# Performance work log

Hardware: AMD Instinct MI355X
Metric: run time of the kernel (lower is better)

Reference implementation:

```python
import jax, jax.numpy as jnp
import numpy as np

B, R, VIS, MM, E, ATT, D, V, MAXLEN = 128, 36, 2048, 1024, 512, 512, 1024, 10000, 20


def setup_inputs() -> dict:
    key = jax.random.key(0)
    ks = jax.random.split(key, 16)
    s = 0.02
    visual = jax.random.normal(ks[0], (B, R, VIS), jnp.float32)
    joint = jax.random.normal(ks[1], (B, MM), jnp.float32)
    captions = jax.random.randint(ks[2], (B, MAXLEN), 0, V)
    # torch code requires lengths sorted descending (prefix slicing)
    lengths = jnp.sort(jax.random.randint(ks[3], (B,), 1, MAXLEN + 1))[::-1].astype(jnp.int32)
    embed_W = (jax.random.normal(ks[4], (V, E), jnp.float32) * s).at[0].set(0.0)  # padding_idx=0
    Wih = jax.random.normal(ks[5], (4 * D, E + VIS), jnp.float32) * s
    bih = jnp.zeros((4 * D,), jnp.float32)
    Whh = jax.random.normal(ks[6], (4 * D, D), jnp.float32) * s
    bhh = jnp.zeros((4 * D,), jnp.float32)
    W_init_h = jax.random.normal(ks[7], (D, MM), jnp.float32) * s
    b_init_h = jnp.zeros((D,), jnp.float32)
    W_init_c = jax.random.normal(ks[8], (D, MM), jnp.float32) * s
    b_init_c = jnp.zeros((D,), jnp.float32)
    Wv = jax.random.normal(ks[9], (ATT, VIS), jnp.float32) * s
    Wh = jax.random.normal(ks[10], (ATT, D), jnp.float32) * s
    att_bias = jnp.zeros((R,), jnp.float32)
    Ww = jax.random.normal(ks[11], (1, ATT), jnp.float32) * s
    Wout = jax.random.normal(ks[12], (V, D), jnp.float32) * s
    bout = jnp.zeros((V,), jnp.float32)
    return dict(visual=visual, joint=joint, captions=captions, lengths=lengths, max_len=MAXLEN,
                embed_W=embed_W, Wih=Wih, bih=bih, Whh=Whh, bhh=bhh,
                W_init_h=W_init_h, b_init_h=b_init_h, W_init_c=W_init_c, b_init_c=b_init_c,
                Wv=Wv, Wh=Wh, att_bias=att_bias, Ww=Ww, Wout=Wout, bout=bout)


def reference(visual, joint, captions, lengths, max_len, embed_W, Wih, bih, Whh, bhh,
              W_init_h, b_init_h, W_init_c, b_init_c, Wv, Wh, att_bias, Ww, Wout, bout):
    T = max_len - 1  # python int -> static scan length
    # dropout treated as identity (eval mode)
    words_seq = embed_W[captions[:, :T]]            # [B, T, E]
    h0 = joint @ W_init_h.T + b_init_h              # [B, D]
    c0 = joint @ W_init_c.T + b_init_c
    feas0 = visual.mean(axis=1)                     # [B, VIS]  (step 0 context)
    att_fea = jnp.einsum('brv,av->bra', visual, Wv)  # precompute visual projection
    lens = lengths.astype(jnp.int32)

    def step(carry, xs):
        h, c = carry
        t, words = xs
        # attention over 36 regions (used only when t != 0)
        ah = h @ Wh.T                                                   # [B, A]
        full = jax.nn.relu(att_fea + ah[:, None, :] + att_bias[None, :, None])
        alpha = jax.nn.softmax(jnp.einsum('bra,a->br', full, Ww[0]), axis=-1)
        ctx = jnp.einsum('br,brv->bv', alpha, visual)
        feas = jnp.where(t == 0, feas0, ctx)
        x = jnp.concatenate([feas, words], axis=-1)                     # [B, VIS+E]
        gates = x @ Wih.T + bih + h @ Whh.T + bhh                       # [B, 4D]
        i_, f_, g_, o_ = jnp.split(gates, 4, axis=-1)
        c_new = jax.nn.sigmoid(f_) * c + jax.nn.sigmoid(i_) * jnp.tanh(g_)
        h_new = jax.nn.sigmoid(o_) * jnp.tanh(c_new)
        mask = (t < lens)[:, None]                                      # ragged mask == torch prefix slice
        out = h_new @ Wout.T + bout                                     # [B, V]
        return (jnp.where(mask, h_new, h), jnp.where(mask, c_new, c)), jnp.where(mask, out, 0.0)

    _, preds = jax.lax.scan(step, (h0, c0), (jnp.arange(T), jnp.swapaxes(words_seq, 0, 1)))
    return jnp.transpose(preds, (1, 0, 2))  # [B, T, V]
```

## Files before the change

### kernel.cpp

```cpp
#include <hip/hip_runtime.h>
#include <math.h>

#define B 128
#define R 36
#define VIS 2048
#define MM 1024
#define E 512
#define ATT 512
#define D 1024
#define V 10000
#define MAXLEN 20
#define T 19
#define G4 4096

typedef unsigned short bf16_t;
typedef __attribute__((ext_vector_type(8))) short short8;
typedef __attribute__((ext_vector_type(4))) float f32x4;
typedef __attribute__((ext_vector_type(4))) unsigned short ushort4v;

__device__ __forceinline__ bf16_t f2bf(float f) {
    unsigned u = __float_as_uint(f);
    u += 0x7fff + ((u >> 16) & 1);
    return (bf16_t)(u >> 16);
}
__device__ __forceinline__ float bf2f(bf16_t b) {
    return __uint_as_float(((unsigned)b) << 16);
}
__device__ __forceinline__ float sigmoidf_(float x) { return 1.0f / (1.0f + expf(-x)); }

__device__ __forceinline__ void stage16(const bf16_t* g, bf16_t* lds_wave_base, int lane) {
#if defined(__has_builtin) && __has_builtin(__builtin_amdgcn_global_load_lds)
    __builtin_amdgcn_global_load_lds(
        (const __attribute__((address_space(1))) void*)g,
        (__attribute__((address_space(3))) void*)lds_wave_base, 16, 0, 0);
#else
    *(short8*)(lds_wave_base + lane * 8) = *(const short8*)g;
#endif
}

template<int MODE>
__global__ __launch_bounds__(256) void mfma_gemm_lds(
    const bf16_t* __restrict__ A, const bf16_t* __restrict__ W,
    const float* __restrict__ bias, const int* __restrict__ lengths,
    float* __restrict__ C, int M, int N, int K, int ldc)
{
    __shared__ __align__(16) bf16_t As[128 * 32];
    __shared__ __align__(16) bf16_t Ws[128 * 32];
    const int tid = threadIdx.x;
    const int wave = tid >> 6, lane = tid & 63;
    const int wm = wave >> 1, wn = wave & 1;
    const int quad = lane >> 4, l16 = lane & 15;
    const int m0 = blockIdx.y * 128;
    const int n0 = blockIdx.x * 128;
    if (MODE == 2 && n0 >= N) return;

    int cnt = 128;
    if constexpr (MODE == 2) {
        const int tt = blockIdx.y;
        cnt = __syncthreads_count(tid < B && lengths[tid] > tt);
    }

    f32x4 acc[4][4];
    #pragma unroll
    for (int i = 0; i < 4; ++i)
        #pragma unroll
        for (int j = 0; j < 4; ++j)
            acc[i][j] = (f32x4){0.f, 0.f, 0.f, 0.f};

    for (int kk = 0; kk < K; kk += 32) {
        #pragma unroll
        for (int i = 0; i < 2; ++i) {
            int c = tid + i * 256;
            int row = c >> 2, seg = c & 3;
            int m = m0 + row; if (m >= M) m = M - 1;
            stage16(A + (size_t)m * K + kk + seg * 8, &As[(i * 256 + wave * 64) * 8], lane);
            int n = n0 + row; if (n >= N) n = N - 1;
            stage16(W + (size_t)n * K + kk + seg * 8, &Ws[(i * 256 + wave * 64) * 8], lane);
        }
        __syncthreads();
        short8 af[4], bfr[4];
        #pragma unroll
        for (int fm = 0; fm < 4; ++fm) {
            const int rt = (MODE == 2) ? fm * 2 + wm : wm * 4 + fm;
            if (MODE != 2 || rt * 16 < cnt)
                af[fm] = *(const short8*)&As[(rt * 16 + l16) * 32 + quad * 8];
        }
        #pragma unroll
        for (int fn = 0; fn < 4; ++fn)
            bfr[fn] = *(const short8*)&Ws[(wn * 64 + fn * 16 + l16) * 32 + quad * 8];
        #pragma unroll
        for (int fm = 0; fm < 4; ++fm) {
            const int rt = (MODE == 2) ? fm * 2 + wm : wm * 4 + fm;
            if (MODE == 2 && rt * 16 >= cnt) continue;
            #pragma unroll
            for (int fn = 0; fn < 4; ++fn)
                acc[fm][fn] = __builtin_amdgcn_mfma_f32_16x16x32_bf16(
                    af[fm], bfr[fn], acc[fm][fn], 0, 0, 0);
        }
        __syncthreads();
    }

    #pragma unroll
    for (int fm = 0; fm < 4; ++fm) {
        const int rt = (MODE == 2) ? fm * 2 + wm : wm * 4 + fm;
        #pragma unroll
        for (int fn = 0; fn < 4; ++fn) {
            #pragma unroll
            for (int r = 0; r < 4; ++r) {
                int m = m0 + rt * 16 + quad * 4 + r;
                int n = n0 + wn * 64 + fn * 16 + l16;
                if (m >= M || n >= N) continue;
                float v = acc[fm][fn][r];
                if (MODE == 0) {
                    if (bias) v += bias[n];
                    C[(size_t)m * ldc + n] = v;
                } else if (MODE == 2) {
                    int t = m >> 7, b = m & 127;
                    v = (t < lengths[b]) ? (v + bias[n]) : 0.f;
                    C[((size_t)b * T + t) * V + n] = v;
                } else {
                    ((bf16_t*)C)[(size_t)m * ldc + n] = f2bf(v);
                }
            }
        }
    }
}

__global__ __launch_bounds__(256) void gemv_ah(
    const float* __restrict__ hf, const bf16_t* __restrict__ Wh_bf,
    float* __restrict__ ah)
{
    __shared__ float hs[16 * D];
    const int tid = threadIdx.x;
    const int bg = blockIdx.x;
    const int ag = blockIdx.y;
    const float4* src = (const float4*)(hf + (size_t)bg * 16 * D);
    #pragma unroll
    for (int i = 0; i < 16; ++i)
        ((float4*)hs)[i * 256 + tid] = src[i * 256 + tid];
    __syncthreads();

    const int lane = tid & 63, wave = tid >> 6;
    const int a = ag * 64 + lane;
    const bf16_t* wr = Wh_bf + (size_t)a * D;
    const float* h0 = hs + (wave * 4 + 0) * D;
    const float* h1 = hs + (wave * 4 + 1) * D;
    const float* h2 = hs + (wave * 4 + 2) * D;
    const float* h3 = hs + (wave * 4 + 3) * D;
    float s0 = 0.f, s1 = 0.f, s2 = 0.f, s3 = 0.f;
    for (int k = 0; k < D; k += 8) {
        short8 wv = *(const short8*)(wr + k);
        #pragma unroll
        for (int j = 0; j < 8; ++j) {
            float w = bf2f((bf16_t)wv[j]);
            s0 = fmaf(w, h0[k + j], s0);
            s1 = fmaf(w, h1[k + j], s1);
            s2 = fmaf(w, h2[k + j], s2);
            s3 = fmaf(w, h3[k + j], s3);
        }
    }
    const int b = bg * 16 + wave * 4;
    ah[(size_t)(b + 0) * ATT + a] = s0;
    ah[(size_t)(b + 1) * ATT + a] = s1;
    ah[(size_t)(b + 2) * ATT + a] = s2;
    ah[(size_t)(b + 3) * ATT + a] = s3;
}

__global__ __launch_bounds__(256) void att_sc_p(
    const float* __restrict__ ah, const float* __restrict__ att_fea,
    const float* __restrict__ att_bias, const float* __restrict__ Ww,
    const bf16_t* __restrict__ P_bf, const float* __restrict__ wordsW,
    float* __restrict__ partial, int t)
{
    const int b = blockIdx.x, half = blockIdx.y, tid = threadIdx.x;
    __shared__ float ah_s[ATT];
    __shared__ float sc_s[64];
    __shared__ float alpha_s[R];
    const int wave = tid >> 6, lane = tid & 63;

    if (t > 0) {
        if (tid < 128) ((float4*)ah_s)[tid] = ((const float4*)(ah + (size_t)b * ATT))[tid];
        __syncthreads();
        for (int r = wave; r < R; r += 4) {
            float abv = att_bias[r];
            const float* af = att_fea + ((size_t)b * R + r) * ATT;
            float s = 0.f;
            for (int a = lane; a < ATT; a += 64) {
                float v = af[a] + ah_s[a] + abv;
                s = fmaf(fmaxf(v, 0.f), Ww[a], s);
            }
            #pragma unroll
            for (int off = 32; off; off >>= 1) s += __shfl_down(s, off);
            if (lane == 0) sc_s[r] = s;
        }
        __syncthreads();
        if (tid < 64) {
            float v = (tid < R) ? sc_s[tid] : -INFINITY;
            float m = v;
            #pragma unroll
            for (int off = 32; off; off >>= 1) m = fmaxf(m, __shfl_down(m, off));
            m = __shfl(m, 0);
            float e = (tid < R) ? expf(v - m) : 0.f;
            float ss = e;
            #pragma unroll
            for (int off = 32; off; off >>= 1) ss += __shfl_down(ss, off);
            ss = __shfl(ss, 0);
            if (tid < R) alpha_s[tid] = e / ss;
        }
        __syncthreads();
    }

    const int n0c = half * 2048 + tid * 8;
    float acc[8];
    #pragma unroll
    for (int j = 0; j < 8; ++j) acc[j] = 0.f;
    const bf16_t* Pb = P_bf + (size_t)b * R * G4 + n0c;
    #pragma unroll 4
    for (int r = 0; r < R; ++r) {
        float al = (t == 0) ? (1.0f / R) : alpha_s[r];
        short8 p = *(const short8*)(Pb + (size_t)r * G4);
        #pragma unroll
        for (int j = 0; j < 8; ++j)
            acc[j] = fmaf(al, bf2f((bf16_t)p[j]), acc[j]);
    }
    const float* wsl = wordsW + ((size_t)t * B + b) * G4 + n0c;
    float* po = partial + (size_t)b * G4 + n0c;
    float4 w0 = *(const float4*)(wsl);
    float4 w1 = *(const float4*)(wsl + 4);
    float4 o0 = { acc[0] + w0.x, acc[1] + w0.y, acc[2] + w0.z, acc[3] + w0.w };
    float4 o1 = { acc[4] + w1.x, acc[5] + w1.y, acc[6] + w1.z, acc[7] + w1.w };
    *(float4*)(po)     = o0;
    *(float4*)(po + 4) = o1;
}

__global__ __launch_bounds__(256) void whh_pack_k(
    const bf16_t* __restrict__ Whh, bf16_t* __restrict__ pk)
{
    int idx = blockIdx.x * 256 + threadIdx.x;
    int dt = idx >> 12, c = idx & 4095;
    int row = c & 31, qk = c >> 5;
    int rv = (row >> 3) * D + dt * 8 + (row & 7);
    *(short8*)(pk + ((size_t)dt << 15) + (size_t)c * 8) =
        *(const short8*)(Whh + (size_t)rv * D + qk * 8);
}

__global__ __launch_bounds__(256) void gates_lstm(
    const bf16_t* __restrict__ h_in,
    const bf16_t* __restrict__ Whh_pk,
    const float* __restrict__ bih, const float* __restrict__ bhh,
    const float* __restrict__ partial,
    const int* __restrict__ lengths,
    float* __restrict__ c_st,
    float* __restrict__ h_f32,
    bf16_t* __restrict__ h_out,
    bf16_t* __restrict__ hseq,
    int t)
{
    __shared__ __align__(16) bf16_t Ws[32 * 1024];
    const int tid = threadIdx.x;
    const int wave = tid >> 6, lane = tid & 63;
    const int quad = lane >> 4, l16 = lane & 15;
    const int d0 = blockIdx.x * 8;
    const int m0 = blockIdx.y * 64;
    const int gsel_ = l16 >> 3, dr = l16 & 7;

    const bf16_t* slab = Whh_pk + ((size_t)blockIdx.x << 15);
    #pragma unroll
    for (int i = 0; i < 16; ++i) {
        int c = i * 256 + tid;
        stage16(slab + (size_t)c * 8, &Ws[(i * 256 + wave * 64) * 8], lane);
    }

    const bf16_t* Ar = h_in + (size_t)(m0 + wave * 16 + l16) * D + quad * 8;

    f32x4 acc0 = (f32x4){0.f, 0.f, 0.f, 0.f};
    f32x4 acc1 = (f32x4){0.f, 0.f, 0.f, 0.f};
    __syncthreads();

    #pragma unroll 8
    for (int kt = 0; kt < 32; ++kt) {
        short8 af = *(const short8*)(Ar + kt * 32);
        const int cb = (kt * 4 + quad) * 32 * 8;
        short8 b0 = *(const short8*)&Ws[cb + l16 * 8];
        short8 b1 = *(const short8*)&Ws[cb + (16 + l16) * 8];
        acc0 = __builtin_amdgcn_mfma_f32_16x16x32_bf16(af, b0, acc0, 0, 0, 0);
        acc1 = __builtin_amdgcn_mfma_f32_16x16x32_bf16(af, b1, acc1, 0, 0, 0);
    }

    const int d = d0 + dr;
    const int col0 = gsel_ * D + d;
    const int col1 = (2 + gsel_) * D + d;
    const float bia0 = bih[col0] + bhh[col0];
    const float bia1 = bih[col1] + bhh[col1];

    #pragma unroll
    for (int r = 0; r < 4; ++r) {
        int m = m0 + wave * 16 + quad * 4 + r;
        size_t pb = (size_t)m * G4;
        float v0 = acc0[r] + bia0 + partial[pb + col0];
        float v1 = acc1[r] + bia1 + partial[pb + col1];
        float w0 = __shfl_xor(v0, 8);
        float w1 = __shfl_xor(v1, 8);
        float iv, fv, gv, ov;
        if (gsel_ == 0) { iv = v0; gv = v1; fv = w0; ov = w1; }
        else            { fv = v0; ov = v1; iv = w0; gv = w1; }
        float ig = sigmoidf_(iv), fg = sigmoidf_(fv);
        float gg = tanhf(gv),     og = sigmoidf_(ov);
        size_t off = (size_t)m * D + d;
        if (gsel_ == 0) {
            float c_old = c_st[off];
            float h_old = h_f32[off];
            float cn = fmaf(fg, c_old, ig * gg);
            float hn = og * tanhf(cn);
            bool msk = t < lengths[m];
            float cv = msk ? cn : c_old;
            float hv = msk ? hn : h_old;
            c_st[off] = cv;
            h_f32[off] = hv;
            bf16_t hb = f2bf(hv);
            h_out[off] = hb;
            hseq[((size_t)t * B + m) * D + d] = hb;
        }
    }
}

__global__ __launch_bounds__(256) void cast_bf16_k(
    const float* __restrict__ src, bf16_t* __restrict__ dst,
    int rows, int cols, int ld)
{
    int idx = blockIdx.x * 256 + threadIdx.x;
    int total = rows * (cols >> 2);
    if (idx >= total) return;
    int cq = cols >> 2;
    int r = idx / cq, c4 = (idx - r * cq) * 4;
    float4 v = *(const float4*)(src + (size_t)r * ld + c4);
    ushort4v o = { f2bf(v.x), f2bf(v.y), f2bf(v.z), f2bf(v.w) };
    *(ushort4v*)(dst + (size_t)r * cols + c4) = o;
}

__global__ __launch_bounds__(128) void embed_k(
    const int* __restrict__ captions, const float* __restrict__ embed_W,
    bf16_t* __restrict__ words_bf)
{
    int bt = blockIdx.x;
    int b = bt / T, t = bt - b * T;
    int tok = captions[b * MAXLEN + t];
    int i = threadIdx.x * 4;
    float4 v = *(const float4*)(embed_W + (size_t)tok * E + i);
    ushort4v o = { f2bf(v.x), f2bf(v.y), f2bf(v.z), f2bf(v.w) };
    *(ushort4v*)(words_bf + ((size_t)t * B + b) * E + i) = o;
}

extern "C" void kernel_launch(void* const* d_in, const int* in_sizes, int n_in,
                              void* d_out, int out_size, void* d_ws, size_t ws_size,
                              hipStream_t stream) {
    const float* visual   = (const float*)d_in[0];
    const float* joint    = (const float*)d_in[1];
    const int*   captions = (const int*)d_in[2];
    const int*   lengths  = (const int*)d_in[3];
    const float* embed_W  = (const float*)d_in[5];
    const float* Wih      = (const float*)d_in[6];
    const float* bih      = (const float*)d_in[7];
    const float* Whh      = (const float*)d_in[8];
    const float* bhh      = (const float*)d_in[9];
    const float* W_init_h = (const float*)d_in[10];
    const float* b_init_h = (const float*)d_in[11];
    const float* W_init_c = (const float*)d_in[12];
    const float* b_init_c = (const float*)d_in[13];
    const float* Wv       = (const float*)d_in[14];
    const float* Wh       = (const float*)d_in[15];
    const float* att_bias = (const float*)d_in[16];
    const float* Ww       = (const float*)d_in[17];
    const float* Wout     = (const float*)d_in[18];
    const float* bout     = (const float*)d_in[19];
    float* out = (float*)d_out;

    char* cur = (char*)d_ws;
    auto alloc = [&](size_t bytes) { char* p = cur; cur += (bytes + 15) & ~size_t(15); return p; };
    float*  att_fea  = (float*)alloc((size_t)B * R * ATT * 4);
    float*  wordsW   = (float*)alloc((size_t)T * B * G4 * 4);
    float*  partial  = (float*)alloc((size_t)B * G4 * 4);
    float*  hf       = (float*)alloc((size_t)B * D * 4);
    float*  c_st     = (float*)alloc((size_t)B * D * 4);
    float*  ah       = (float*)alloc((size_t)B * ATT * 4);
    bf16_t* words_bf = (bf16_t*)alloc((size_t)T * B * E * 2);
    bf16_t* h_ping0  = (bf16_t*)alloc((size_t)B * D * 2);
    bf16_t* h_ping1  = (bf16_t*)alloc((size_t)B * D * 2);
    bf16_t* hseq_bf  = (bf16_t*)alloc((size_t)T * B * D * 2);
    bf16_t* P_bf     = (bf16_t*)alloc((size_t)B * R * G4 * 2);
    bf16_t* visual_bf= (bf16_t*)alloc((size_t)B * R * VIS * 2);
    bf16_t* Wv_bf    = (bf16_t*)alloc((size_t)ATT * VIS * 2);
    bf16_t* Wh_bf    = (bf16_t*)alloc((size_t)ATT * D * 2);
    bf16_t* Whh_bf   = (bf16_t*)alloc((size_t)G4 * D * 2);
    bf16_t* Whh_pk   = (bf16_t*)alloc((size_t)G4 * D * 2);
    bf16_t* Wih_v_bf = (bf16_t*)alloc((size_t)G4 * VIS * 2);
    bf16_t* Wih_w_bf = (bf16_t*)alloc((size_t)G4 * E * 2);
    bf16_t* Wout_bf  = (bf16_t*)alloc((size_t)V * D * 2);
    bf16_t* joint_bf = (bf16_t*)alloc((size_t)B * MM * 2);
    bf16_t* Winh_bf  = (bf16_t*)alloc((size_t)D * MM * 2);
    bf16_t* Winc_bf  = (bf16_t*)alloc((size_t)D * MM * 2);

    auto cast = [&](const float* s, bf16_t* dst, int rows, int cols, int ld) {
        int total = rows * (cols >> 2);
        cast_bf16_k<<<(total + 255) / 256, 256, 0, stream>>>(s, dst, rows, cols, ld);
    };
    cast(visual, visual_bf, 1, B * R * VIS, B * R * VIS);
    cast(Wv,  Wv_bf,  ATT, VIS, VIS);
    cast(Wh,  Wh_bf,  ATT, D, D);
    cast(Whh, Whh_bf, G4, D, D);
    cast(Wih, Wih_v_bf, G4, VIS, VIS + E);
    cast(Wih + VIS, Wih_w_bf, G4, E, VIS + E);
    cast(Wout, Wout_bf, V, D, D);
    cast(joint, joint_bf, 1, B * MM, B * MM);
    cast(W_init_h, Winh_bf, 1, D * MM, D * MM);
    cast(W_init_c, Winc_bf, 1, D * MM, D * MM);

    whh_pack_k<<<(128 * 4096) / 256, 256, 0, stream>>>(Whh_bf, Whh_pk);
    embed_k<<<B * T, 128, 0, stream>>>(captions, embed_W, words_bf);

    mfma_gemm_lds<0><<<dim3(D / 128, B / 128), 256, 0, stream>>>(
        joint_bf, Winh_bf, b_init_h, nullptr, hf, B, D, MM, D);
    mfma_gemm_lds<0><<<dim3(D / 128, B / 128), 256, 0, stream>>>(
        joint_bf, Winc_bf, b_init_c, nullptr, c_st, B, D, MM, D);
    cast(hf, h_ping0, 1, B * D, B * D);

    mfma_gemm_lds<0><<<dim3(ATT / 128, (B * R) / 128), 256, 0, stream>>>(
        visual_bf, Wv_bf, nullptr, nullptr, att_fea, B * R, ATT, VIS, ATT);

    mfma_gemm_lds<0><<<dim3(G4 / 128, (T * B) / 128), 256, 0, stream>>>(
        words_bf, Wih_w_bf, nullptr, nullptr, wordsW, T * B, G4, E, G4);

    mfma_gemm_lds<3><<<dim3(G4 / 128, (B * R) / 128), 256, 0, stream>>>(
        visual_bf, Wih_v_bf, nullptr, nullptr, (float*)P_bf, B * R, G4, VIS, G4);

    bf16_t* h_buf[2] = { h_ping0, h_ping1 };
    for (int t = 0; t < T; ++t) {
        if (t > 0)
            gemv_ah<<<dim3(8, 8), 256, 0, stream>>>(hf, Wh_bf, ah);
        att_sc_p<<<dim3(B, 2), 256, 0, stream>>>(
            ah, att_fea, att_bias, Ww, P_bf, wordsW, partial, t);
        gates_lstm<<<dim3(D / 8, B / 64), 256, 0, stream>>>(
            h_buf[t & 1], Whh_pk, bih, bhh, partial, lengths,
            c_st, hf, h_buf[(t + 1) & 1], hseq_bf, t);
    }

    mfma_gemm_lds<2><<<dim3(80, (T * B) / 128), 256, 0, stream>>>(
        hseq_bf, Wout_bf, bout, lengths, out, T * B, V, D, V);
}
```

Baseline: 1.534 ms.

## Use MFMA for attention hidden projection, fuse casts and init GEMMs

Replaces the scalar fp32 gemv for h@Wh^T with an MFMA bf16 kernel that reads a pre-packed Wh slab staged into LDS and the bf16 hidden state directly. The ten cast launches become one fused cast kernel. The two init GEMMs for h0/c0 become one GEMM that also writes the bf16 copy of h0. The output GEMM skips staging A rows that the length mask zeroes anyway. These target per-step latency in the recurrent loop and launch overhead, at the cost of bf16 rounding of h in the attention projection.

Measured after the change: 1.269 ms. 17.3% less time.

```diff
diff --git a/kernel.cpp b/kernel.cpp
--- a/kernel.cpp
+++ b/kernel.cpp
@@ -42,7 +42,9 @@
 __global__ __launch_bounds__(256) void mfma_gemm_lds(
     const bf16_t* __restrict__ A, const bf16_t* __restrict__ W,
     const float* __restrict__ bias, const int* __restrict__ lengths,
-    float* __restrict__ C, int M, int N, int K, int ldc)
+    float* __restrict__ C, int M, int N, int K, int ldc,
+    const float* __restrict__ bias2, float* __restrict__ C2,
+    bf16_t* __restrict__ C3)
 {
     __shared__ __align__(16) bf16_t As[128 * 32];
     __shared__ __align__(16) bf16_t Ws[128 * 32];
@@ -72,8 +74,10 @@
         for (int i = 0; i < 2; ++i) {
             int c = tid + i * 256;
             int row = c >> 2, seg = c & 3;
-            int m = m0 + row; if (m >= M) m = M - 1;
-            stage16(A + (size_t)m * K + kk + seg * 8, &As[(i * 256 + wave * 64) * 8], lane);
+            if (MODE != 2 || (i * 64 + wave * 16) < cnt) {
+                int m = m0 + row; if (m >= M) m = M - 1;
+                stage16(A + (size_t)m * K + kk + seg * 8, &As[(i * 256 + wave * 64) * 8], lane);
+            }
             int n = n0 + row; if (n >= N) n = N - 1;
             stage16(W + (size_t)n * K + kk + seg * 8, &Ws[(i * 256 + wave * 64) * 8], lane);
         }
@@ -118,6 +122,14 @@
                     int t = m >> 7, b = m & 127;
                     v = (t < lengths[b]) ? (v + bias[n]) : 0.f;
                     C[((size_t)b * T + t) * V + n] = v;
+                } else if (MODE == 4) {
+                    if (n < D) {
+                        float v2 = v + bias[n];
+                        C[(size_t)m * D + n] = v2;
+                        C3[(size_t)m * D + n] = f2bf(v2);
+                    } else {
+                        C2[(size_t)m * D + (n - D)] = v + bias2[n - D];
+                    }
                 } else {
                     ((bf16_t*)C)[(size_t)m * ldc + n] = f2bf(v);
                 }
@@ -126,44 +138,44 @@
     }
 }
 
-__global__ __launch_bounds__(256) void gemv_ah(
-    const float* __restrict__ hf, const bf16_t* __restrict__ Wh_bf,
+__global__ __launch_bounds__(256) void mfma_ah(
+    const bf16_t* __restrict__ h_in,
+    const bf16_t* __restrict__ Wh_pk,
     float* __restrict__ ah)
 {
-    __shared__ float hs[16 * D];
+    __shared__ __align__(16) bf16_t Ws[32 * 1024];
     const int tid = threadIdx.x;
-    const int bg = blockIdx.x;
-    const int ag = blockIdx.y;
-    const float4* src = (const float4*)(hf + (size_t)bg * 16 * D);
-    #pragma unroll
-    for (int i = 0; i < 16; ++i)
-        ((float4*)hs)[i * 256 + tid] = src[i * 256 + tid];
+    const int wave = tid >> 6, lane = tid & 63;
+    const int quad = lane >> 4, l16 = lane & 15;
+    const int a0 = blockIdx.x * 32;
+    const int m0 = blockIdx.y * 64;
+
+    const bf16_t* slab = Wh_pk + ((size_t)blockIdx.x << 15);
+    #pragma unroll
+    for (int i = 0; i < 16; ++i) {
+        int c = i * 256 + tid;
+        stage16(slab + (size_t)c * 8, &Ws[(i * 256 + wave * 64) * 8], lane);
+    }
+    const bf16_t* Ar = h_in + (size_t)(m0 + wave * 16 + l16) * D + quad * 8;
+    f32x4 acc0 = (f32x4){0.f, 0.f, 0.f, 0.f};
+    f32x4 acc1 = (f32x4){0.f, 0.f, 0.f, 0.f};
     __syncthreads();
 
-    const int lane = tid & 63, wave = tid >> 6;
-    const int a = ag * 64 + lane;
-    const bf16_t* wr = Wh_bf + (size_t)a * D;
-    const float* h0 = hs + (wave * 4 + 0) * D;
-    const float* h1 = hs + (wave * 4 + 1) * D;
-    const float* h2 = hs + (wave * 4 + 2) * D;
-    const float* h3 = hs + (wave * 4 + 3) * D;
-    float s0 = 0.f, s1 = 0.f, s2 = 0.f, s3 = 0.f;
-    for (int k = 0; k < D; k += 8) {
-        short8 wv = *(const short8*)(wr + k);
-        #pragma unroll
-        for (int j = 0; j < 8; ++j) {
-            float w = bf2f((bf16_t)wv[j]);
-            s0 = fmaf(w, h0[k + j], s0);
-            s1 = fmaf(w, h1[k + j], s1);
-            s2 = fmaf(w, h2[k + j], s2);
-            s3 = fmaf(w, h3[k + j], s3);
-        }
-    }
-    const int b = bg * 16 + wave * 4;
-    ah[(size_t)(b + 0) * ATT + a] = s0;
-    ah[(size_t)(b + 1) * ATT + a] = s1;
-    ah[(size_t)(b + 2) * ATT + a] = s2;
-    ah[(size_t)(b + 3) * ATT + a] = s3;
+    #pragma unroll 8
+    for (int kt = 0; kt < 32; ++kt) {
+        short8 af = *(const short8*)(Ar + kt * 32);
+        const int cb = (kt * 4 + quad) * 32 * 8;
+        short8 b0 = *(const short8*)&Ws[cb + l16 * 8];
+        short8 b1 = *(const short8*)&Ws[cb + (16 + l16) * 8];
+        acc0 = __builtin_amdgcn_mfma_f32_16x16x32_bf16(af, b0, acc0, 0, 0, 0);
+        acc1 = __builtin_amdgcn_mfma_f32_16x16x32_bf16(af, b1, acc1, 0, 0, 0);
+    }
+    #pragma unroll
+    for (int r = 0; r < 4; ++r) {
+        int m = m0 + wave * 16 + quad * 4 + r;
+        ah[(size_t)m * ATT + a0 + l16]      = acc0[r];
+        ah[(size_t)m * ATT + a0 + 16 + l16] = acc1[r];
+    }
 }
 
 __global__ __launch_bounds__(256) void att_sc_p(
@@ -242,6 +254,16 @@
     int rv = (row >> 3) * D + dt * 8 + (row & 7);
     *(short8*)(pk + ((size_t)dt << 15) + (size_t)c * 8) =
         *(const short8*)(Whh + (size_t)rv * D + qk * 8);
+}
+
+__global__ __launch_bounds__(256) void wh_pack_k(
+    const bf16_t* __restrict__ Wh, bf16_t* __restrict__ pk)
+{
+    int idx = blockIdx.x * 256 + threadIdx.x;
+    int at = idx >> 12, c = idx & 4095;
+    int row = c & 31, qk = c >> 5;
+    *(short8*)(pk + ((size_t)at << 15) + (size_t)c * 8) =
+        *(const short8*)(Wh + (size_t)(at * 32 + row) * D + qk * 8);
 }
 
 __global__ __launch_bounds__(256) void gates_lstm(
@@ -324,18 +346,22 @@
     }
 }
 
-__global__ __launch_bounds__(256) void cast_bf16_k(
-    const float* __restrict__ src, bf16_t* __restrict__ dst,
-    int rows, int cols, int ld)
-{
-    int idx = blockIdx.x * 256 + threadIdx.x;
-    int total = rows * (cols >> 2);
-    if (idx >= total) return;
-    int cq = cols >> 2;
+struct CastSeg { const float* s; bf16_t* d; int cols; int ld; int total4; int blk0; };
+struct Cast10 { CastSeg g[10]; };
+
+__global__ __launch_bounds__(256) void fused_cast_k(Cast10 a)
+{
+    const int bx = blockIdx.x;
+    CastSeg sg = a.g[0];
+    #pragma unroll
+    for (int j = 1; j < 10; ++j) if (bx >= a.g[j].blk0) sg = a.g[j];
+    int idx = (bx - sg.blk0) * 256 + threadIdx.x;
+    if (idx >= sg.total4) return;
+    int cq = sg.cols >> 2;
     int r = idx / cq, c4 = (idx - r * cq) * 4;
-    float4 v = *(const float4*)(src + (size_t)r * ld + c4);
+    float4 v = *(const float4*)(sg.s + (size_t)r * sg.ld + c4);
     ushort4v o = { f2bf(v.x), f2bf(v.y), f2bf(v.z), f2bf(v.w) };
-    *(ushort4v*)(dst + (size_t)r * cols + c4) = o;
+    *(ushort4v*)(sg.d + (size_t)r * sg.cols + c4) = o;
 }
 
 __global__ __launch_bounds__(128) void embed_k(
@@ -391,52 +417,59 @@
     bf16_t* visual_bf= (bf16_t*)alloc((size_t)B * R * VIS * 2);
     bf16_t* Wv_bf    = (bf16_t*)alloc((size_t)ATT * VIS * 2);
     bf16_t* Wh_bf    = (bf16_t*)alloc((size_t)ATT * D * 2);
+    bf16_t* Wh_pk    = (bf16_t*)alloc((size_t)ATT * D * 2);
     bf16_t* Whh_bf   = (bf16_t*)alloc((size_t)G4 * D * 2);
     bf16_t* Whh_pk   = (bf16_t*)alloc((size_t)G4 * D * 2);
     bf16_t* Wih_v_bf = (bf16_t*)alloc((size_t)G4 * VIS * 2);
     bf16_t* Wih_w_bf = (bf16_t*)alloc((size_t)G4 * E * 2);
     bf16_t* Wout_bf  = (bf16_t*)alloc((size_t)V * D * 2);
     bf16_t* joint_bf = (bf16_t*)alloc((size_t)B * MM * 2);
-    bf16_t* Winh_bf  = (bf16_t*)alloc((size_t)D * MM * 2);
-    bf16_t* Winc_bf  = (bf16_t*)alloc((size_t)D * MM * 2);
-
-    auto cast = [&](const float* s, bf16_t* dst, int rows, int cols, int ld) {
-        int total = rows * (cols >> 2);
-        cast_bf16_k<<<(total + 255) / 256, 256, 0, stream>>>(s, dst, rows, cols, ld);
+    bf16_t* Winit_bf = (bf16_t*)alloc((size_t)2 * D * MM * 2);
+
+    Cast10 ca;
+    int cum = 0;
+    auto seg = [&](int i, const float* s, bf16_t* d, int rows, int cols, int ld) {
+        int t4 = rows * (cols >> 2);
+        ca.g[i] = { s, d, cols, ld, t4, cum };
+        cum += (t4 + 255) / 256;
     };
-    cast(visual, visual_bf, 1, B * R * VIS, B * R * VIS);
-    cast(Wv,  Wv_bf,  ATT, VIS, VIS);
-    cast(Wh,  Wh_bf,  ATT, D, D);
-    cast(Whh, Whh_bf, G4, D, D);
-    cast(Wih, Wih_v_bf, G4, VIS, VIS + E);
-    cast(Wih + VIS, Wih_w_bf, G4, E, VIS + E);
-    cast(Wout, Wout_bf, V, D, D);
-    cast(joint, joint_bf, 1, B * MM, B * MM);
-    cast(W_init_h, Winh_bf, 1, D * MM, D * MM);
-    cast(W_init_c, Winc_bf, 1, D * MM, D * MM);
+    seg(0, visual, visual_bf, 1, B * R * VIS, B * R * VIS);
+    seg(1, Wv,  Wv_bf,  ATT, VIS, VIS);
+    seg(2, Wh,  Wh_bf,  ATT, D, D);
+    seg(3, Whh, Whh_bf, G4, D, D);
+    seg(4, Wih, Wih_v_bf, G4, VIS, VIS + E);
+    seg(5, Wih + VIS, Wih_w_bf, G4, E, VIS + E);
+    seg(6, Wout, Wout_bf, V, D, D);
+    seg(7, joint, joint_bf, 1, B * MM, B * MM);
+    seg(8, W_init_h, Winit_bf, 1, D * MM, D * MM);
+    seg(9, W_init_c, Winit_bf + (size_t)D * MM, 1, D * MM, D * MM);
+    fused_cast_k<<<cum, 256, 0, stream>>>(ca);
 
     whh_pack_k<<<(128 * 4096) / 256, 256, 0, stream>>>(Whh_bf, Whh_pk);
+    wh_pack_k<<<(16 * 4096) / 256, 256, 0, stream>>>(Wh_bf, Wh_pk);
     embed_k<<<B * T, 128, 0, stream>>>(captions, embed_W, words_bf);
 
-    mfma_gemm_lds<0><<<dim3(D / 128, B / 128), 256, 0, stream>>>(
-        joint_bf, Winh_bf, b_init_h, nullptr, hf, B, D, MM, D);
-    mfma_gemm_lds<0><<<dim3(D / 128, B / 128), 256, 0, stream>>>(
-        joint_bf, Winc_bf, b_init_c, nullptr, c_st, B, D, MM, D);
-    cast(hf, h_ping0, 1, B * D, B * D);
+    mfma_gemm_lds<4><<<dim3(16, 1), 256, 0, stream>>>(
+        joint_bf, Winit_bf, b_init_h, nullptr, hf, B, 2 * D, MM, D,
+        b_init_c, c_st, h_ping0);
 
     mfma_gemm_lds<0><<<dim3(ATT / 128, (B * R) / 128), 256, 0, stream>>>(
-        visual_bf, Wv_bf, nullptr, nullptr, att_fea, B * R, ATT, VIS, ATT);
+        visual_bf, Wv_bf, nullptr, nullptr, att_fea, B * R, ATT, VIS, ATT,
+        nullptr, nullptr, nullptr);
 
     mfma_gemm_lds<0><<<dim3(G4 / 128, (T * B) / 128), 256, 0, stream>>>(
-        words_bf, Wih_w_bf, nullptr, nullptr, wordsW, T * B, G4, E, G4);
+        words_bf, Wih_w_bf, nullptr, nullptr, wordsW, T * B, G4, E, G4,
+        nullptr, nullptr, nullptr);
 
     mfma_gemm_lds<3><<<dim3(G4 / 128, (B * R) / 128), 256, 0, stream>>>(
-        visual_bf, Wih_v_bf, nullptr, nullptr, (float*)P_bf, B * R, G4, VIS, G4);
+        visual_bf, Wih_v_bf, nullptr, nullptr, (float*)P_bf, B * R, G4, VIS, G4,
+        nullptr, nullptr, nullptr);
 
     bf16_t* h_buf[2] = { h_ping0, h_ping1 };
     for (int t = 0; t < T; ++t) {
         if (t > 0)
-            gemv_ah<<<dim3(8, 8), 256, 0, stream>>>(hf, Wh_bf, ah);
+            mfma_ah<<<dim3(ATT / 32, B / 64), 256, 0, stream>>>(
+                h_buf[t & 1], Wh_pk, ah);
         att_sc_p<<<dim3(B, 2), 256, 0, stream>>>(
             ah, att_fea, att_bias, Ww, P_bf, wordsW, partial, t);
         gates_lstm<<<dim3(D / 8, B / 64), 256, 0, stream>>>(
@@ -445,5 +478,6 @@
     }
 
     mfma_gemm_lds<2><<<dim3(80, (T * B) / 128), 256, 0, stream>>>(
-        hseq_bf, Wout_bf, bout, lengths, out, T * B, V, D, V);
-}
+        hseq_bf, Wout_bf, bout, lengths, out, T * B, V, D, V,
+        nullptr, nullptr, nullptr);
+}
```
